# Performance work log

Hardware: AMD Instinct MI355X
Metric: run time of the kernel (lower is better)

## Reference

```python
import jax, jax.numpy as jnp
import numpy as np

B, T, C, H = 2, 2048, 1024, 16
HS = C // H  # head size = 64


def _rope_cos_sin(t, hs):
    # theta_i = 1/10000^(2(i-1)/hs) for i in [1, hs/2]
    pos = jnp.arange(t, dtype=jnp.float32)[:, None]          # [T,1]
    i = jnp.arange(1, hs // 2 + 1, dtype=jnp.float32)[None]  # [1,hs/2]
    theta = 1.0 / 10000.0 ** (2.0 * (i - 1.0) / hs)
    ang = pos * theta                                        # [T,hs/2]
    return jnp.cos(ang), jnp.sin(ang)


def _apply_rope(u, cos, sin):
    # u: [B,H,T,HS]; complex multiply on consecutive pairs
    u2 = u.reshape(*u.shape[:-1], HS // 2, 2)
    x0, x1 = u2[..., 0], u2[..., 1]
    c = cos[None, None]  # [1,1,T,hs/2]
    s = sin[None, None]
    r0 = x0 * c - x1 * s
    r1 = x0 * s + x1 * c
    return jnp.stack([r0, r1], axis=-1).reshape(u.shape)


def setup_inputs() -> dict:
    key = jax.random.key(0)
    ks = jax.random.split(key, 5)
    return {
        "x": jax.random.normal(ks[0], (B, T, C), dtype=jnp.float32),
        "W_qkv": jax.random.normal(ks[1], (C, 3 * C), dtype=jnp.float32) * 0.02,
        "b_qkv": jax.random.normal(ks[2], (3 * C,), dtype=jnp.float32) * 0.02,
        "W_proj": jax.random.normal(ks[3], (C, C), dtype=jnp.float32) * 0.02,
        "b_proj": jax.random.normal(ks[4], (C,), dtype=jnp.float32) * 0.02,
    }


def reference(x, W_qkv, b_qkv, W_proj, b_proj):
    b, t, c = x.shape
    qkv = x @ W_qkv + b_qkv                                   # [B,T,3C]
    qkv = qkv.reshape(b, t, H, 3 * HS).transpose(0, 2, 1, 3)  # [B,H,T,3*HS]
    q, k, v = jnp.split(qkv, 3, axis=-1)                      # each [B,H,T,HS]

    cos, sin = _rope_cos_sin(t, HS)
    q = _apply_rope(q, cos, sin)
    k = _apply_rope(k, cos, sin)

    att = jnp.einsum("bhqd,bhkd->bhqk", q, k) / jnp.sqrt(jnp.float32(HS))
    causal = jnp.tril(jnp.ones((t, t), dtype=bool))[None, None]
    att = jnp.where(causal, att, jnp.float32(-1e9))
    att = jax.nn.softmax(att, axis=-1)
    y = jnp.einsum("bhqk,bhkd->bhqd", att, v)                 # [B,H,T,HS]
    y = y.transpose(0, 2, 1, 3).reshape(b, t, c)
    return y @ W_proj + b_proj
```

## Files before the change

kernel.cpp:

```cpp
#include <hip/hip_runtime.h>

typedef unsigned short u16;
typedef unsigned int u32;
typedef __bf16 bf16x8 __attribute__((ext_vector_type(8)));
typedef float f32x4 __attribute__((ext_vector_type(4)));
typedef u16 u16x4 __attribute__((ext_vector_type(4)));
typedef u16 u16x8 __attribute__((ext_vector_type(8)));

__device__ __forceinline__ u16 f2bf(float f) {
  u32 u = __builtin_bit_cast(u32, f);
  u += 0x7fffu + ((u >> 16) & 1u);
  return (u16)(u >> 16);
}

__device__ __forceinline__ u32 pk2(float a, float b) {
  u32 ua = __builtin_bit_cast(u32, a) + 0x8000u;
  u32 ub = __builtin_bit_cast(u32, b) + 0x8000u;
  return __builtin_amdgcn_perm(ub, ua, 0x07060302);
}

__device__ __forceinline__ void gld16(const void* g, void* l) {
  __builtin_amdgcn_global_load_lds(
      (const __attribute__((address_space(1))) void*)g,
      (__attribute__((address_space(3))) void*)l, 16, 0, 0);
}

__global__ __launch_bounds__(256) void k_prep(
    const float* __restrict__ x, u16* __restrict__ xb,
    const float* __restrict__ Wqkv, u16* __restrict__ Wqkvt,
    const float* __restrict__ Wproj, u16* __restrict__ Wpt,
    float2* __restrict__ rope) {
  __shared__ float tile[32][33];
  const int tid = threadIdx.x;
  int bx = blockIdx.x;
  if (bx < 4096) {
    int i = (bx * 256 + tid) * 4;
    float4 v = *(const float4*)(x + i);
    u16x4 o = { f2bf(v.x), f2bf(v.y), f2bf(v.z), f2bf(v.w) };
    *(u16x4*)(xb + i) = o;
    return;
  }
  bx -= 4096;
  const float* src; u16* dst; int R, Cc, bxx, byy;
  if (bx < 3072) {
    src = Wqkv; dst = Wqkvt; R = 1024; Cc = 3072; bxx = bx % 96; byy = bx / 96;
  } else if (bx < 4096) {
    int b = bx - 3072;
    src = Wproj; dst = Wpt; R = 1024; Cc = 1024; bxx = b % 32; byy = b / 32;
  } else {
    int i = (bx - 4096) * 256 + tid;
    int t = i >> 5, d = i & 31;
    float theta = expf(-(float)d * 0.28782313662425575f);
    float ang = (float)t * theta;
    rope[i] = make_float2(cosf(ang), sinf(ang));
    return;
  }
  int xx = tid & 31, yy = tid >> 5;
  int c0 = bxx * 32, r0 = byy * 32;
  for (int i = 0; i < 4; ++i)
    tile[yy + 8 * i][xx] = src[(size_t)(r0 + yy + 8 * i) * Cc + c0 + xx];
  __syncthreads();
  for (int i = 0; i < 4; ++i)
    dst[(size_t)(c0 + yy + 8 * i) * R + r0 + xx] = f2bf(tile[xx][yy + 8 * i]);
}

__global__ __launch_bounds__(256) void k_qkv(
    const u16* __restrict__ Xb,
    const u16* __restrict__ Wt,
    const float* __restrict__ bias,
    const float2* __restrict__ rope,
    u16* __restrict__ Qg,
    u16* __restrict__ Kg,
    u16* __restrict__ Vt) {
  __shared__ alignas(16) u16 As[128 * 32];
  __shared__ alignas(16) u16 Bs[128 * 32];
  __shared__ alignas(16) u16 Es[2][9216];
  const int tid = threadIdx.x;
  const int lane = tid & 63, w = tid >> 6;
  const int quad = lane >> 4, l15 = lane & 15;
  const int m0 = blockIdx.y * 128, n0 = blockIdx.x * 128;
  const int lr = lane >> 2, lc = (lane & 3) * 8;
  const int wm = (w & 1) * 64, wn = (w >> 1) * 64;
  const f32x4 vzero = {0.f, 0.f, 0.f, 0.f};

  const int half = w >> 1;
  const int nh = n0 + half * 64;
  const int region = (nh % 192) >> 6;
  const bool swapped = (region < 2);

  f32x4 acc[4][4];
  for (int i = 0; i < 4; ++i)
    for (int j = 0; j < 4; ++j) acc[i][j] = vzero;

  for (int kt = 0; kt < 1024; kt += 32) {
    __syncthreads();
    for (int i = 0; i < 2; ++i) {
      int row = w * 32 + i * 16;
      gld16(Xb + (size_t)(m0 + row + lr) * 1024 + kt + lc, &As[row * 32]);
      gld16(Wt + (size_t)(n0 + row + lr) * 1024 + kt + lc, &Bs[row * 32]);
    }
    __syncthreads();
    bf16x8 a[4], b[4];
    for (int mt = 0; mt < 4; ++mt)
      a[mt] = *(const bf16x8*)&As[(wm + mt * 16 + l15) * 32 + quad * 8];
    for (int nt = 0; nt < 4; ++nt)
      b[nt] = *(const bf16x8*)&Bs[(wn + nt * 16 + l15) * 32 + quad * 8];
    if (swapped) {
      for (int nt = 0; nt < 4; ++nt)
        for (int mt = 0; mt < 4; ++mt)
          acc[nt][mt] = __builtin_amdgcn_mfma_f32_16x16x32_bf16(
              b[nt], a[mt], acc[nt][mt], 0, 0, 0);
    } else {
      for (int mt = 0; mt < 4; ++mt)
        for (int nt = 0; nt < 4; ++nt)
          acc[mt][nt] = __builtin_amdgcn_mfma_f32_16x16x32_bf16(
              a[mt], b[nt], acc[mt][nt], 0, 0, 0);
    }
  }

  if (swapped) {
    for (int nt = 0; nt < 4; ++nt) {
      float4 bv4 = *(const float4*)&bias[nh + nt * 16 + quad * 4];
      for (int mt = 0; mt < 4; ++mt) {
        int m_l = wm + mt * 16 + l15;
        int t = (m0 + m_l) & 2047;
        float4 cs = *(const float4*)&rope[t * 32 + nt * 8 + quad * 2];
        float v0 = acc[nt][mt][0] + bv4.x;
        float v1 = acc[nt][mt][1] + bv4.y;
        float v2 = acc[nt][mt][2] + bv4.z;
        float v3 = acc[nt][mt][3] + bv4.w;
        float r0 = fmaf(-v1, cs.y, v0 * cs.x);
        float r1 = fmaf( v0, cs.y, v1 * cs.x);
        float r2 = fmaf(-v3, cs.w, v2 * cs.z);
        float r3 = fmaf( v2, cs.w, v3 * cs.z);
        uint2 pv; pv.x = pk2(r0, r1); pv.y = pk2(r2, r3);
        *(uint2*)&Es[half][m_l * 72 + nt * 16 + quad * 4] = pv;
      }
    }
  } else {
    for (int nt = 0; nt < 4; ++nt) {
      int c = nt * 16 + l15;
      float bv = bias[nh + c];
      for (int mt = 0; mt < 4; ++mt) {
        float v0 = acc[mt][nt][0] + bv, v1 = acc[mt][nt][1] + bv;
        float v2 = acc[mt][nt][2] + bv, v3 = acc[mt][nt][3] + bv;
        uint2 pv; pv.x = pk2(v0, v1); pv.y = pk2(v2, v3);
        *(uint2*)&Es[half][c * 136 + wm + mt * 16 + quad * 4] = pv;
      }
    }
  }
  __syncthreads();

  const int bb = m0 >> 11, t0 = m0 & 2047;
  for (int hf = 0; hf < 2; ++hf) {
    const int nhf = n0 + hf * 64;
    const int hh = nhf / 192;
    const int reg = (nhf % 192) >> 6;
    if (reg < 2) {
      u16* dst = (reg == 0 ? Qg : Kg) +
                 ((size_t)(bb * 16 + hh) * 2048 + t0) * 64;
      int chunk = tid & 7, row0 = tid >> 3;
      for (int p = 0; p < 4; ++p) {
        int row = row0 + p * 32;
        u16x8 val = *(const u16x8*)&Es[hf][row * 72 + chunk * 8];
        *(u16x8*)(dst + (size_t)row * 64 + chunk * 8) = val;
      }
    } else {
      u16* dstv = Vt + (size_t)(bb * 16 + hh) * 64 * 2048 + t0;
      int mch = tid & 15, c0r = tid >> 4;
      for (int p = 0; p < 4; ++p) {
        int c = c0r + p * 16;
        u16x8 val = *(const u16x8*)&Es[hf][c * 136 + mch * 8];
        *(u16x8*)(dstv + (size_t)c * 2048 + mch * 8) = val;
      }
    }
  }
}

__global__ __launch_bounds__(512, 4) void k_attn(
    const u16* __restrict__ Qg, const u16* __restrict__ Kg,
    const u16* __restrict__ Vt, u16* __restrict__ Og) {
  __shared__ alignas(16) u16 Ks[2][64 * 64];
  __shared__ alignas(16) u16 Vs[2][64 * 64];
  __shared__ alignas(16) u16 Ps[128 * 72];
  const int tid = threadIdx.x, lane = tid & 63, w = tid >> 6;
  const int quad = lane >> 4, l15 = lane & 15;
  const int bh = blockIdx.y;
  int tmp = (blockIdx.x + bh) & 15;
  const int qt = (bh & 16) ? (15 - tmp) : tmp;
  const int q0 = qt * 128;
  const u16* Qh = Qg + (size_t)bh * 2048 * 64;
  const u16* Kh = Kg + (size_t)bh * 2048 * 64;
  const u16* Vh = Vt + (size_t)bh * 64 * 2048;
  const f32x4 vzero = {0.f, 0.f, 0.f, 0.f};
  const float SCL = 0.125f * 1.4426950408889634f;
  const int myrow = w * 16;

  bf16x8 aq[2];
  {
    const u16* qp = Qh + (size_t)(q0 + myrow + l15) * 64 + quad * 8;
    aq[0] = *(const bf16x8*)(qp);
    aq[1] = *(const bf16x8*)(qp + 32);
  }

  const int r8 = lane >> 3, j8 = lane & 7;
  const int sw_c = (j8 ^ r8) * 8;

  float lsum = 0.f;
  f32x4 O[4];
  for (int nt = 0; nt < 4; ++nt) O[nt] = vzero;

  const int nk = 2 * qt + 2;
  gld16(Kh + (size_t)(w * 8 + r8) * 64 + sw_c, &Ks[0][w * 8 * 64]);
  gld16(Vh + (size_t)(w * 8 + r8) * 2048 + sw_c, &Vs[0][w * 8 * 64]);

  for (int kb = 0; kb < nk; ++kb) {
    const int k0 = kb * 64;
    const int cur = kb & 1;
    __syncthreads();
    if (kb + 1 < nk) {
      const int k1 = k0 + 64;
      gld16(Kh + (size_t)(k1 + w * 8 + r8) * 64 + sw_c, &Ks[cur ^ 1][w * 8 * 64]);
      gld16(Vh + (size_t)(w * 8 + r8) * 2048 + k1 + sw_c, &Vs[cur ^ 1][w * 8 * 64]);
    }
    if (k0 > q0 + myrow + 15) continue;

    f32x4 st[4];
    for (int nt = 0; nt < 4; ++nt) st[nt] = vzero;
    for (int ks = 0; ks < 2; ++ks) {
      bf16x8 ak[4];
      for (int nt = 0; nt < 4; ++nt)
        ak[nt] = *(const bf16x8*)&Ks[cur][(nt * 16 + l15) * 64 +
                                         ((ks * 4 + quad) ^ (l15 & 7)) * 8];
      for (int nt = 0; nt < 4; ++nt)
        st[nt] = __builtin_amdgcn_mfma_f32_16x16x32_bf16(ak[nt], aq[ks], st[nt], 0, 0, 0);
    }

    if (k0 + 63 <= q0 + myrow) {
      for (int nt = 0; nt < 4; ++nt) {
        float p0 = __builtin_amdgcn_exp2f(st[nt][0] * SCL);
        float p1 = __builtin_amdgcn_exp2f(st[nt][1] * SCL);
        float p2 = __builtin_amdgcn_exp2f(st[nt][2] * SCL);
        float p3 = __builtin_amdgcn_exp2f(st[nt][3] * SCL);
        lsum += (p0 + p1) + (p2 + p3);
        uint2 pv; pv.x = pk2(p0, p1); pv.y = pk2(p2, p3);
        *(uint2*)&Ps[(myrow + l15) * 72 + nt * 16 + quad * 4] = pv;
      }
    } else {
      const int tq = q0 + myrow + l15;
      const int kbase = k0 + quad * 4;
      for (int nt = 0; nt < 4; ++nt) {
        float p[4];
        for (int r = 0; r < 4; ++r) {
          float pv = __builtin_amdgcn_exp2f(st[nt][r] * SCL);
          p[r] = (kbase + nt * 16 + r <= tq) ? pv : 0.f;
          lsum += p[r];
        }
        uint2 pv; pv.x = pk2(p[0], p[1]); pv.y = pk2(p[2], p[3]);
        *(uint2*)&Ps[(myrow + l15) * 72 + nt * 16 + quad * 4] = pv;
      }
    }

    for (int ks = 0; ks < 2; ++ks) {
      bf16x8 a = *(const bf16x8*)&Ps[(myrow + l15) * 72 + ks * 32 + quad * 8];
      bf16x8 bv[4];
      for (int nt = 0; nt < 4; ++nt)
        bv[nt] = *(const bf16x8*)&Vs[cur][(nt * 16 + l15) * 64 +
                                         ((ks * 4 + quad) ^ (l15 & 7)) * 8];
      for (int nt = 0; nt < 4; ++nt)
        O[nt] = __builtin_amdgcn_mfma_f32_16x16x32_bf16(a, bv[nt], O[nt], 0, 0, 0);
    }
  }

  lsum += __shfl_xor(lsum, 16, 64);
  lsum += __shfl_xor(lsum, 32, 64);
  float inv[4];
  for (int r = 0; r < 4; ++r)
    inv[r] = 1.0f / __shfl(lsum, quad * 4 + r, 16);

  for (int nt = 0; nt < 4; ++nt)
    for (int r = 0; r < 4; ++r)
      Ps[(myrow + quad * 4 + r) * 72 + nt * 16 + l15] = f2bf(O[nt][r] * inv[r]);
  __syncthreads();
  const int bb = bh >> 4, h = bh & 15;
  u16* dst = Og + ((size_t)bb * 2048 + q0) * 1024 + h * 64;
  int chunk = tid & 7, row0 = tid >> 3;
  for (int p = 0; p < 2; ++p) {
    int row = row0 + p * 64;
    u16x8 val = *(const u16x8*)&Ps[row * 72 + chunk * 8];
    *(u16x8*)(dst + (size_t)row * 1024 + chunk * 8) = val;
  }
}

__global__ __launch_bounds__(256) void k_proj(
    const u16* __restrict__ Ag,
    const u16* __restrict__ Wt,
    const float* __restrict__ bias,
    float* __restrict__ out) {
  __shared__ alignas(16) u16 As[128 * 32];
  __shared__ alignas(16) u16 Bs[128 * 32];
  const int tid = threadIdx.x;
  const int lane = tid & 63, w = tid >> 6;
  const int quad = lane >> 4, l15 = lane & 15;
  const int m0 = blockIdx.y * 128, n0 = blockIdx.x * 128;
  const int lr = lane >> 2, lc = (lane & 3) * 8;
  const int wm = (w & 1) * 64, wn = (w >> 1) * 64;
  const f32x4 vzero = {0.f, 0.f, 0.f, 0.f};

  f32x4 acc[4][4];
  for (int i = 0; i < 4; ++i)
    for (int j = 0; j < 4; ++j) acc[i][j] = vzero;

  for (int kt = 0; kt < 1024; kt += 32) {
    __syncthreads();
    for (int i = 0; i < 2; ++i) {
      int row = w * 32 + i * 16;
      gld16(Ag + (size_t)(m0 + row + lr) * 1024 + kt + lc, &As[row * 32]);
      gld16(Wt + (size_t)(n0 + row + lr) * 1024 + kt + lc, &Bs[row * 32]);
    }
    __syncthreads();
    bf16x8 a[4], b[4];
    for (int mt = 0; mt < 4; ++mt)
      a[mt] = *(const bf16x8*)&As[(wm + mt * 16 + l15) * 32 + quad * 8];
    for (int nt = 0; nt < 4; ++nt)
      b[nt] = *(const bf16x8*)&Bs[(wn + nt * 16 + l15) * 32 + quad * 8];
    for (int mt = 0; mt < 4; ++mt)
      for (int nt = 0; nt < 4; ++nt)
        acc[mt][nt] = __builtin_amdgcn_mfma_f32_16x16x32_bf16(
            a[mt], b[nt], acc[mt][nt], 0, 0, 0);
  }

  for (int nt = 0; nt < 4; ++nt) {
    int n = n0 + wn + nt * 16 + l15;
    float bv = bias[n];
    for (int mt = 0; mt < 4; ++mt)
      for (int r = 0; r < 4; ++r) {
        int m = m0 + wm + mt * 16 + quad * 4 + r;
        out[(size_t)m * 1024 + n] = acc[mt][nt][r] + bv;
      }
  }
}

extern "C" void kernel_launch(void* const* d_in, const int* in_sizes, int n_in,
                              void* d_out, int out_size, void* d_ws, size_t ws_size,
                              hipStream_t stream) {
  (void)in_sizes; (void)n_in; (void)out_size; (void)ws_size;
  const float* x     = (const float*)d_in[0];
  const float* Wqkv  = (const float*)d_in[1];
  const float* bqkv  = (const float*)d_in[2];
  const float* Wproj = (const float*)d_in[3];
  const float* bproj = (const float*)d_in[4];
  float* out = (float*)d_out;

  char* ws = (char*)d_ws;
  size_t off = 0;
  u16* Xb    = (u16*)(ws + off); off += (size_t)4096 * 1024 * 2;
  u16* Wqkvt = (u16*)(ws + off); off += (size_t)3072 * 1024 * 2;
  u16* Wpt   = (u16*)(ws + off); off += (size_t)1024 * 1024 * 2;
  u16* Qg    = (u16*)(ws + off); off += (size_t)2 * 16 * 2048 * 64 * 2;
  u16* Kg    = (u16*)(ws + off); off += (size_t)2 * 16 * 2048 * 64 * 2;
  u16* Vt    = (u16*)(ws + off); off += (size_t)2 * 16 * 64 * 2048 * 2;
  u16* Att   = (u16*)(ws + off); off += (size_t)4096 * 1024 * 2;
  float2* rope = (float2*)(ws + off); off += (size_t)2048 * 32 * sizeof(float2);

  k_prep<<<8448, 256, 0, stream>>>(x, Xb, Wqkv, Wqkvt, Wproj, Wpt, rope);
  k_qkv<<<dim3(24, 32), 256, 0, stream>>>(Xb, Wqkvt, bqkv, rope, Qg, Kg, Vt);
  k_attn<<<dim3(16, 32), 512, 0, stream>>>(Qg, Kg, Vt, Att);
  k_proj<<<dim3(8, 32), 256, 0, stream>>>(Att, Wpt, bproj, out);
}
```

Before: 196.4 us.

## Use K=64 XOR-swizzled LDS tiles in QKV/proj GEMMs and halve proj M-tile

The QKV and projection GEMMs now stage 64-wide K slices with an XOR swizzle, so LDS reads avoid bank conflicts and the loop runs half as many barrier-separated iterations. The QKV kernel aliases its epilogue staging buffer onto the A/B tile memory to cut shared-memory use and adds an occupancy hint. It also always uses the swapped MFMA operand order, so the V path writes scalar transposed stores instead. The projection kernel uses 64-row M tiles, doubling the grid to 512 blocks for better CU fill, at the cost of less B-tile reuse per block.

```diff
diff --git a/kernel.cpp b/kernel.cpp
--- a/kernel.cpp
+++ b/kernel.cpp
@@ -64,7 +64,7 @@
     dst[(size_t)(c0 + yy + 8 * i) * R + r0 + xx] = f2bf(tile[xx][yy + 8 * i]);
 }
 
-__global__ __launch_bounds__(256) void k_qkv(
+__global__ __launch_bounds__(256, 4) void k_qkv(
     const u16* __restrict__ Xb,
     const u16* __restrict__ Wt,
     const float* __restrict__ bias,
@@ -72,53 +72,50 @@
     u16* __restrict__ Qg,
     u16* __restrict__ Kg,
     u16* __restrict__ Vt) {
-  __shared__ alignas(16) u16 As[128 * 32];
-  __shared__ alignas(16) u16 Bs[128 * 32];
-  __shared__ alignas(16) u16 Es[2][9216];
+  __shared__ alignas(16) u16 smem[18432];
+  u16* As = smem;
+  u16* Bs = smem + 8192;
   const int tid = threadIdx.x;
   const int lane = tid & 63, w = tid >> 6;
   const int quad = lane >> 4, l15 = lane & 15;
   const int m0 = blockIdx.y * 128, n0 = blockIdx.x * 128;
-  const int lr = lane >> 2, lc = (lane & 3) * 8;
   const int wm = (w & 1) * 64, wn = (w >> 1) * 64;
+  const int srow = lane >> 3, sj = lane & 7;
+  const int sw = (sj ^ srow) * 8;
   const f32x4 vzero = {0.f, 0.f, 0.f, 0.f};
+
+  f32x4 acc[4][4];
+  for (int i = 0; i < 4; ++i)
+    for (int j = 0; j < 4; ++j) acc[i][j] = vzero;
+
+  for (int kt = 0; kt < 1024; kt += 64) {
+    __syncthreads();
+    for (int i = 0; i < 4; ++i) {
+      int row = w * 32 + i * 8;
+      gld16(Xb + (size_t)(m0 + row + srow) * 1024 + kt + sw, &As[row * 64]);
+      gld16(Wt + (size_t)(n0 + row + srow) * 1024 + kt + sw, &Bs[row * 64]);
+    }
+    __syncthreads();
+    for (int ks = 0; ks < 2; ++ks) {
+      const int cc = ((ks * 4 + quad) ^ (l15 & 7)) * 8;
+      bf16x8 a[4], b[4];
+      for (int mt = 0; mt < 4; ++mt)
+        a[mt] = *(const bf16x8*)&As[(wm + mt * 16 + l15) * 64 + cc];
+      for (int nt = 0; nt < 4; ++nt)
+        b[nt] = *(const bf16x8*)&Bs[(wn + nt * 16 + l15) * 64 + cc];
+      for (int nt = 0; nt < 4; ++nt)
+        for (int mt = 0; mt < 4; ++mt)
+          acc[nt][mt] = __builtin_amdgcn_mfma_f32_16x16x32_bf16(
+              b[nt], a[mt], acc[nt][mt], 0, 0, 0);
+    }
+  }
+  __syncthreads();
 
   const int half = w >> 1;
   const int nh = n0 + half * 64;
   const int region = (nh % 192) >> 6;
-  const bool swapped = (region < 2);
-
-  f32x4 acc[4][4];
-  for (int i = 0; i < 4; ++i)
-    for (int j = 0; j < 4; ++j) acc[i][j] = vzero;
-
-  for (int kt = 0; kt < 1024; kt += 32) {
-    __syncthreads();
-    for (int i = 0; i < 2; ++i) {
-      int row = w * 32 + i * 16;
-      gld16(Xb + (size_t)(m0 + row + lr) * 1024 + kt + lc, &As[row * 32]);
-      gld16(Wt + (size_t)(n0 + row + lr) * 1024 + kt + lc, &Bs[row * 32]);
-    }
-    __syncthreads();
-    bf16x8 a[4], b[4];
-    for (int mt = 0; mt < 4; ++mt)
-      a[mt] = *(const bf16x8*)&As[(wm + mt * 16 + l15) * 32 + quad * 8];
-    for (int nt = 0; nt < 4; ++nt)
-      b[nt] = *(const bf16x8*)&Bs[(wn + nt * 16 + l15) * 32 + quad * 8];
-    if (swapped) {
-      for (int nt = 0; nt < 4; ++nt)
-        for (int mt = 0; mt < 4; ++mt)
-          acc[nt][mt] = __builtin_amdgcn_mfma_f32_16x16x32_bf16(
-              b[nt], a[mt], acc[nt][mt], 0, 0, 0);
-    } else {
-      for (int mt = 0; mt < 4; ++mt)
-        for (int nt = 0; nt < 4; ++nt)
-          acc[mt][nt] = __builtin_amdgcn_mfma_f32_16x16x32_bf16(
-              a[mt], b[nt], acc[mt][nt], 0, 0, 0);
-    }
-  }
-
-  if (swapped) {
+  u16* Eh = smem + half * 9216;
+  if (region < 2) {
     for (int nt = 0; nt < 4; ++nt) {
       float4 bv4 = *(const float4*)&bias[nh + nt * 16 + quad * 4];
       for (int mt = 0; mt < 4; ++mt) {
@@ -134,18 +131,19 @@
         float r2 = fmaf(-v3, cs.w, v2 * cs.z);
         float r3 = fmaf( v2, cs.w, v3 * cs.z);
         uint2 pv; pv.x = pk2(r0, r1); pv.y = pk2(r2, r3);
-        *(uint2*)&Es[half][m_l * 72 + nt * 16 + quad * 4] = pv;
+        *(uint2*)&Eh[m_l * 72 + nt * 16 + quad * 4] = pv;
       }
     }
   } else {
     for (int nt = 0; nt < 4; ++nt) {
-      int c = nt * 16 + l15;
-      float bv = bias[nh + c];
+      float4 bv4 = *(const float4*)&bias[nh + nt * 16 + quad * 4];
       for (int mt = 0; mt < 4; ++mt) {
-        float v0 = acc[mt][nt][0] + bv, v1 = acc[mt][nt][1] + bv;
-        float v2 = acc[mt][nt][2] + bv, v3 = acc[mt][nt][3] + bv;
-        uint2 pv; pv.x = pk2(v0, v1); pv.y = pk2(v2, v3);
-        *(uint2*)&Es[half][c * 136 + wm + mt * 16 + quad * 4] = pv;
+        int m_l = wm + mt * 16 + l15;
+        int cb = nt * 16 + quad * 4;
+        Eh[(cb + 0) * 136 + m_l] = f2bf(acc[nt][mt][0] + bv4.x);
+        Eh[(cb + 1) * 136 + m_l] = f2bf(acc[nt][mt][1] + bv4.y);
+        Eh[(cb + 2) * 136 + m_l] = f2bf(acc[nt][mt][2] + bv4.z);
+        Eh[(cb + 3) * 136 + m_l] = f2bf(acc[nt][mt][3] + bv4.w);
       }
     }
   }
@@ -156,13 +154,14 @@
     const int nhf = n0 + hf * 64;
     const int hh = nhf / 192;
     const int reg = (nhf % 192) >> 6;
+    const u16* Ef = smem + hf * 9216;
     if (reg < 2) {
       u16* dst = (reg == 0 ? Qg : Kg) +
                  ((size_t)(bb * 16 + hh) * 2048 + t0) * 64;
       int chunk = tid & 7, row0 = tid >> 3;
       for (int p = 0; p < 4; ++p) {
         int row = row0 + p * 32;
-        u16x8 val = *(const u16x8*)&Es[hf][row * 72 + chunk * 8];
+        u16x8 val = *(const u16x8*)&Ef[row * 72 + chunk * 8];
         *(u16x8*)(dst + (size_t)row * 64 + chunk * 8) = val;
       }
     } else {
@@ -170,7 +169,7 @@
       int mch = tid & 15, c0r = tid >> 4;
       for (int p = 0; p < 4; ++p) {
         int c = c0r + p * 16;
-        u16x8 val = *(const u16x8*)&Es[hf][c * 136 + mch * 8];
+        u16x8 val = *(const u16x8*)&Ef[c * 136 + mch * 8];
         *(u16x8*)(dstv + (size_t)c * 2048 + mch * 8) = val;
       }
     }
@@ -292,48 +291,55 @@
   }
 }
 
-__global__ __launch_bounds__(256) void k_proj(
+__global__ __launch_bounds__(256, 4) void k_proj(
     const u16* __restrict__ Ag,
     const u16* __restrict__ Wt,
     const float* __restrict__ bias,
     float* __restrict__ out) {
-  __shared__ alignas(16) u16 As[128 * 32];
-  __shared__ alignas(16) u16 Bs[128 * 32];
+  __shared__ alignas(16) u16 As[64 * 64];
+  __shared__ alignas(16) u16 Bs[128 * 64];
   const int tid = threadIdx.x;
   const int lane = tid & 63, w = tid >> 6;
   const int quad = lane >> 4, l15 = lane & 15;
-  const int m0 = blockIdx.y * 128, n0 = blockIdx.x * 128;
-  const int lr = lane >> 2, lc = (lane & 3) * 8;
-  const int wm = (w & 1) * 64, wn = (w >> 1) * 64;
+  const int m0 = blockIdx.y * 64, n0 = blockIdx.x * 128;
+  const int wm = (w & 1) * 32, wn = (w >> 1) * 64;
+  const int srow = lane >> 3, sj = lane & 7;
+  const int sw = (sj ^ srow) * 8;
   const f32x4 vzero = {0.f, 0.f, 0.f, 0.f};
 
-  f32x4 acc[4][4];
-  for (int i = 0; i < 4; ++i)
+  f32x4 acc[2][4];
+  for (int i = 0; i < 2; ++i)
     for (int j = 0; j < 4; ++j) acc[i][j] = vzero;
 
-  for (int kt = 0; kt < 1024; kt += 32) {
+  for (int kt = 0; kt < 1024; kt += 64) {
     __syncthreads();
     for (int i = 0; i < 2; ++i) {
-      int row = w * 32 + i * 16;
-      gld16(Ag + (size_t)(m0 + row + lr) * 1024 + kt + lc, &As[row * 32]);
-      gld16(Wt + (size_t)(n0 + row + lr) * 1024 + kt + lc, &Bs[row * 32]);
-    }
-    __syncthreads();
-    bf16x8 a[4], b[4];
-    for (int mt = 0; mt < 4; ++mt)
-      a[mt] = *(const bf16x8*)&As[(wm + mt * 16 + l15) * 32 + quad * 8];
-    for (int nt = 0; nt < 4; ++nt)
-      b[nt] = *(const bf16x8*)&Bs[(wn + nt * 16 + l15) * 32 + quad * 8];
-    for (int mt = 0; mt < 4; ++mt)
-      for (int nt = 0; nt < 4; ++nt)
-        acc[mt][nt] = __builtin_amdgcn_mfma_f32_16x16x32_bf16(
-            a[mt], b[nt], acc[mt][nt], 0, 0, 0);
+      int row = w * 16 + i * 8;
+      gld16(Ag + (size_t)(m0 + row + srow) * 1024 + kt + sw, &As[row * 64]);
+    }
+    for (int i = 0; i < 4; ++i) {
+      int row = w * 32 + i * 8;
+      gld16(Wt + (size_t)(n0 + row + srow) * 1024 + kt + sw, &Bs[row * 64]);
+    }
+    __syncthreads();
+    for (int ks = 0; ks < 2; ++ks) {
+      const int cc = ((ks * 4 + quad) ^ (l15 & 7)) * 8;
+      bf16x8 a[2], b[4];
+      for (int mt = 0; mt < 2; ++mt)
+        a[mt] = *(const bf16x8*)&As[(wm + mt * 16 + l15) * 64 + cc];
+      for (int nt = 0; nt < 4; ++nt)
+        b[nt] = *(const bf16x8*)&Bs[(wn + nt * 16 + l15) * 64 + cc];
+      for (int mt = 0; mt < 2; ++mt)
+        for (int nt = 0; nt < 4; ++nt)
+          acc[mt][nt] = __builtin_amdgcn_mfma_f32_16x16x32_bf16(
+              a[mt], b[nt], acc[mt][nt], 0, 0, 0);
+    }
   }
 
   for (int nt = 0; nt < 4; ++nt) {
     int n = n0 + wn + nt * 16 + l15;
     float bv = bias[n];
-    for (int mt = 0; mt < 4; ++mt)
+    for (int mt = 0; mt < 2; ++mt)
       for (int r = 0; r < 4; ++r) {
         int m = m0 + wm + mt * 16 + quad * 4 + r;
         out[(size_t)m * 1024 + n] = acc[mt][nt][r] + bv;
@@ -366,5 +372,5 @@
   k_prep<<<8448, 256, 0, stream>>>(x, Xb, Wqkv, Wqkvt, Wproj, Wpt, rope);
   k_qkv<<<dim3(24, 32), 256, 0, stream>>>(Xb, Wqkvt, bqkv, rope, Qg, Kg, Vt);
   k_attn<<<dim3(16, 32), 512, 0, stream>>>(Qg, Kg, Vt, Att);
-  k_proj<<<dim3(8, 32), 256, 0, stream>>>(Att, Wpt, bproj, out);
-}
+  k_proj<<<dim3(8, 64), 256, 0, stream>>>(Att, Wpt, bproj, out);
+}
```

Result: faster. 174.6 us (-11.1%).
